# Kernel tuning notes

Measured on AMD Instinct MI355X. Metric: run time of the kernel, lower is better.

Reference implementation:

```python
import jax, jax.numpy as jnp
import numpy as np

N = 100000          # nodes
E = 3200000         # edges (avg degree 32)
EPS = 1e-5          # BatchNorm eps
SLOPE = 0.01        # LeakyReLU negative slope


def _glorot(key, shape):
    lim = float(np.sqrt(6.0 / (shape[0] + shape[1])))
    return jax.random.uniform(key, shape, jnp.float32, -lim, lim)


def setup_inputs() -> dict:
    key = jax.random.key(0)
    ks = jax.random.split(key, 8)
    x = jax.random.normal(ks[0], (N, 128), jnp.float32)
    edge_index = jax.random.randint(ks[1], (2, E), 0, N, dtype=jnp.int64)
    W1 = _glorot(ks[2], (128, 256)); b1 = jnp.zeros((256,), jnp.float32)
    W2 = _glorot(ks[3], (256, 512)); b2 = jnp.zeros((512,), jnp.float32)
    g1 = jnp.ones((256,), jnp.float32); be1 = jnp.zeros((256,), jnp.float32)
    g2 = jnp.ones((512,), jnp.float32); be2 = jnp.zeros((512,), jnp.float32)
    Wd1 = _glorot(ks[4], (512, 4096)); bd1 = jnp.zeros((4096,), jnp.float32)
    Wd2 = _glorot(ks[5], (4096, 6)); bd2 = jnp.zeros((6,), jnp.float32)
    return dict(x=x, edge_index=edge_index, W1=W1, b1=b1, W2=W2, b2=b2,
                g1=g1, be1=be1, g2=g2, be2=be2,
                Wd1=Wd1, bd1=bd1, Wd2=Wd2, bd2=bd2)


def gcn_conv(x, src, dst, W, b):
    # PyG GCNConv: x' = D^{-1/2} (A + I) D^{-1/2} (x W) + b
    n = x.shape[0]
    xw = x @ W                                   # [N, out]
    loop = jnp.arange(n, dtype=src.dtype)
    s = jnp.concatenate([src, loop])             # add self-loops
    d = jnp.concatenate([dst, loop])
    deg = jax.ops.segment_sum(jnp.ones_like(d, dtype=x.dtype), d, num_segments=n)
    dinv = jnp.where(deg > 0, jax.lax.rsqrt(deg), 0.0)
    norm = dinv[s] * dinv[d]                     # [E+N]
    out = jax.ops.segment_sum(xw[s] * norm[:, None], d, num_segments=n)
    return out + b


def batchnorm(x, g, b):
    # training-mode BN over node dim, biased variance (as torch)
    m = x.mean(axis=0)
    v = x.var(axis=0)
    return (x - m) * jax.lax.rsqrt(v + EPS) * g + b


def leaky_relu(x):
    return jnp.where(x >= 0, x, SLOPE * x)


def reference(x, edge_index, W1, b1, W2, b2, g1, be1, g2, be2, Wd1, bd1, Wd2, bd2):
    src, dst = edge_index[0], edge_index[1]
    y = leaky_relu(batchnorm(gcn_conv(x, src, dst, W1, b1), g1, be1))
    y = leaky_relu(batchnorm(gcn_conv(y, src, dst, W2, b2), g2, be2))
    y = leaky_relu(y @ Wd1 + bd1)
    y = y @ Wd2 + bd2
    return jax.nn.softmax(y, axis=1)
```

## Files before the change

### kernel.cpp

```cpp
#include <hip/hip_runtime.h>
#include <math.h>

#define LEAKY(t) ((t) >= 0.0f ? (t) : 0.01f * (t))

typedef __attribute__((ext_vector_type(8))) short bf16x8;
typedef __attribute__((ext_vector_type(4))) float f32x4;

static __device__ __forceinline__ float b2f(unsigned short u) {
    return __uint_as_float(((unsigned)u) << 16);
}
static __device__ __forceinline__ unsigned short f2b(float f) {
    unsigned x = __float_as_uint(f);
    unsigned r = (x + 0x7fffu + ((x >> 16) & 1u)) >> 16;
    return (unsigned short)r;
}


__global__ void k_seti(int* __restrict__ p, int v, int n) {
    int i = blockIdx.x * blockDim.x + threadIdx.x;
    int st = gridDim.x * blockDim.x;
    for (; i < n; i += st) p[i] = v;
}

__global__ void k_setf(float* __restrict__ p, float v, int n) {
    int i = blockIdx.x * blockDim.x + threadIdx.x;
    int st = gridDim.x * blockDim.x;
    for (; i < n; i += st) p[i] = v;
}

__global__ void k_stash_b16(const unsigned short* __restrict__ a, int i0, int i1, int i2, int i3,
                            float* __restrict__ dst) {
    if (threadIdx.x == 0 && blockIdx.x == 0) {
        dst[0] = b2f(a[i0]); dst[1] = b2f(a[i1]); dst[2] = b2f(a[i2]); dst[3] = b2f(a[i3]);
    }
}


__global__ void k_cvt(const float* __restrict__ src, unsigned short* __restrict__ dst,
                      long long n4) {
    long long i = (long long)blockIdx.x * blockDim.x + threadIdx.x;
    long long st = (long long)gridDim.x * blockDim.x;
    for (; i < n4; i += st) {
        float4 v = *(const float4*)(src + 4 * i);
        ushort4 o;
        o.x = f2b(v.x); o.y = f2b(v.y); o.z = f2b(v.z); o.w = f2b(v.w);
        *(ushort4*)(dst + 4 * i) = o;
    }
}


__global__ void k_detect(const int* __restrict__ ei, int* __restrict__ flag) {
    __shared__ int nz;
    if (threadIdx.x == 0) nz = 0;
    __syncthreads();
    int acc = 0;
    for (int i = threadIdx.x; i < 1024; i += 256) acc |= ei[2 * i + 1];
    if (acc != 0) atomicOr(&nz, 1);
    __syncthreads();
    if (threadIdx.x == 0) *flag = (nz == 0) ? 1 : 0;
}


__global__ void k_count(const int* __restrict__ ei, int E, int Nn,
                        const int* __restrict__ flag, int* __restrict__ cnt) {
    int f = *flag;
    int i = blockIdx.x * blockDim.x + threadIdx.x;
    int stride = gridDim.x * blockDim.x;
    for (; i < E; i += stride) {
        int d = f ? ei[2 * E + 2 * i] : ei[E + i];
        if ((unsigned)d < (unsigned)Nn) atomicAdd(&cnt[d], 1);
    }
}

__global__ void k_dinv(const int* __restrict__ cnt, float* __restrict__ dinv, int n) {
    int i = blockIdx.x * blockDim.x + threadIdx.x;
    if (i < n) dinv[i] = rsqrtf((float)(cnt[i] + 1));
}

__global__ void k_scan(const int* __restrict__ cnt, int* __restrict__ start, int n) {
    __shared__ int sm[256];
    __shared__ int carry;
    int tid = threadIdx.x;
    if (tid == 0) carry = 0;
    __syncthreads();
    for (int base = 0; base < n; base += 1024) {
        int i0 = base + tid * 4;
        int v0 = (i0 + 0 < n) ? cnt[i0 + 0] : 0;
        int v1 = (i0 + 1 < n) ? cnt[i0 + 1] : 0;
        int v2 = (i0 + 2 < n) ? cnt[i0 + 2] : 0;
        int v3 = (i0 + 3 < n) ? cnt[i0 + 3] : 0;
        int s = v0 + v1 + v2 + v3;
        sm[tid] = s;
        __syncthreads();
        int x = s;
        for (int off = 1; off < 256; off <<= 1) {
            int y = (tid >= off) ? sm[tid - off] : 0;
            __syncthreads();
            x += y;
            sm[tid] = x;
            __syncthreads();
        }
        int e = x - s + carry;
        if (i0 + 0 < n) start[i0 + 0] = e; e += v0;
        if (i0 + 1 < n) start[i0 + 1] = e; e += v1;
        if (i0 + 2 < n) start[i0 + 2] = e; e += v2;
        if (i0 + 3 < n) start[i0 + 3] = e; e += v3;
        __syncthreads();
        if (tid == 255) carry += sm[255];
        __syncthreads();
    }
    if (tid == 0) start[n] = carry;
}

__global__ void k_copy_i32(const int* __restrict__ a, int* __restrict__ b, int n) {
    int i = blockIdx.x * blockDim.x + threadIdx.x;
    if (i < n) b[i] = a[i];
}

__global__ void k_fill(const int* __restrict__ ei, int E, int Nn,
                       const int* __restrict__ flag,
                       int* __restrict__ cursor, int* __restrict__ srcS) {
    int f = *flag;
    int i = blockIdx.x * blockDim.x + threadIdx.x;
    int stride = gridDim.x * blockDim.x;
    for (; i < E; i += stride) {
        int s = f ? ei[2 * i] : ei[i];
        int d = f ? ei[2 * E + 2 * i] : ei[E + i];
        if ((unsigned)d < (unsigned)Nn) {
            int p = atomicAdd(&cursor[d], 1);
            srcS[p] = ((unsigned)s < (unsigned)Nn) ? s : 0;
        }
    }
}


__global__ void k_aggb(const unsigned short* __restrict__ X, const float* __restrict__ dinv,
                       const int* __restrict__ start, const int* __restrict__ srcS,
                       unsigned short* __restrict__ out, int F, int M) {
    int t = threadIdx.x;
    for (int n = blockIdx.x; n < M; n += gridDim.x) {
        float di = dinv[n];
        unsigned v = *(const unsigned*)(X + (size_t)n * F + 2 * t);
        float a0 = b2f((unsigned short)(v & 0xffff)) * di;
        float a1 = b2f((unsigned short)(v >> 16)) * di;
        int j = start[n], e1 = start[n + 1];
        for (; j + 1 < e1; j += 2) {
            int s0 = srcS[j], s1 = srcS[j + 1];
            float w0 = dinv[s0], w1 = dinv[s1];
            unsigned u0 = *(const unsigned*)(X + (size_t)s0 * F + 2 * t);
            unsigned u1 = *(const unsigned*)(X + (size_t)s1 * F + 2 * t);
            a0 += b2f((unsigned short)(u0 & 0xffff)) * w0;
            a1 += b2f((unsigned short)(u0 >> 16)) * w0;
            a0 += b2f((unsigned short)(u1 & 0xffff)) * w1;
            a1 += b2f((unsigned short)(u1 >> 16)) * w1;
        }
        if (j < e1) {
            int s0 = srcS[j];
            float w0 = dinv[s0];
            unsigned u0 = *(const unsigned*)(X + (size_t)s0 * F + 2 * t);
            a0 += b2f((unsigned short)(u0 & 0xffff)) * w0;
            a1 += b2f((unsigned short)(u0 >> 16)) * w0;
        }
        unsigned o = (unsigned)f2b(a0 * di) | ((unsigned)f2b(a1 * di) << 16);
        *(unsigned*)(out + (size_t)n * F + 2 * t) = o;
    }
}


__global__ __launch_bounds__(256, 2)
void k_gemm1(const unsigned short* __restrict__ A, const unsigned short* __restrict__ W1s,
             unsigned short* __restrict__ C, int M) {
    int tid = threadIdx.x;
    int lane = tid & 63, w = tid >> 6;
    int lr = lane & 15, lg = lane >> 4;
    int row0 = blockIdx.x * 64;
    int arow = row0 + w * 16 + lr;
    const unsigned short* Ar = A + (size_t)(arow < M ? arow : (M - 1)) * 128;
    bf16x8 a8[4];
#pragma unroll
    for (int ko = 0; ko < 4; ko++)
        a8[ko] = *(const bf16x8*)(Ar + ko * 32 + lg * 8);
    for (int ct = 0; ct < 16; ct += 2) {
        f32x4 acc0 = {0.f, 0.f, 0.f, 0.f}, acc1 = {0.f, 0.f, 0.f, 0.f};
#pragma unroll
        for (int ko = 0; ko < 4; ko++) {
            const unsigned short* bp = W1s + ((size_t)(ct * 4 + ko) * 64 + lane) * 8;
            bf16x8 b0 = *(const bf16x8*)bp;
            bf16x8 b1 = *(const bf16x8*)(bp + 2048);
            acc0 = __builtin_amdgcn_mfma_f32_16x16x32_bf16(a8[ko], b0, acc0, 0, 0, 0);
            acc1 = __builtin_amdgcn_mfma_f32_16x16x32_bf16(a8[ko], b1, acc1, 0, 0, 0);
        }
        int col = ct * 16 + lr;
#pragma unroll
        for (int i = 0; i < 4; i++) {
            int r = row0 + w * 16 + lg * 4 + i;
            if (r < M) {
                C[(size_t)r * 256 + col] = f2b(acc0[i]);
                C[(size_t)r * 256 + col + 16] = f2b(acc1[i]);
            }
        }
    }
}


__global__ void k_gemm2stats(const unsigned short* __restrict__ T2,
                             const unsigned short* __restrict__ W2s,
                             float* __restrict__ sums, int M) {
    __shared__ float ls[512];
    __shared__ float lq[512];
    int tid = threadIdx.x;
    int lane = tid & 63, w = tid >> 6;
    int lr = lane & 15, lg = lane >> 4;
    int row0 = blockIdx.x * 64;
    for (int i = tid; i < 512; i += 256) { ls[i] = 0.f; lq[i] = 0.f; }
    __syncthreads();

    int arow = row0 + w * 16 + lr;
    bf16x8 a8[8];
    if (arow < M) {
        const unsigned short* T2r = T2 + (size_t)arow * 256;
#pragma unroll
        for (int ko = 0; ko < 8; ko++)
            a8[ko] = *(const bf16x8*)(T2r + ko * 32 + lg * 8);
    } else {
#pragma unroll
        for (int ko = 0; ko < 8; ko++)
            a8[ko] = (bf16x8){0, 0, 0, 0, 0, 0, 0, 0};
    }

    for (int ct = 0; ct < 32; ct += 2) {
        f32x4 acc0 = {0.f, 0.f, 0.f, 0.f}, acc1 = {0.f, 0.f, 0.f, 0.f};
#pragma unroll
        for (int ko = 0; ko < 8; ko++) {
            const unsigned short* bp = W2s + ((size_t)(ct * 8 + ko) * 64 + lane) * 8;
            bf16x8 b0 = *(const bf16x8*)bp;
            bf16x8 b1 = *(const bf16x8*)(bp + 4096);
            acc0 = __builtin_amdgcn_mfma_f32_16x16x32_bf16(a8[ko], b0, acc0, 0, 0, 0);
            acc1 = __builtin_amdgcn_mfma_f32_16x16x32_bf16(a8[ko], b1, acc1, 0, 0, 0);
        }
        float s0 = 0.f, q0 = 0.f, s1 = 0.f, q1 = 0.f;
#pragma unroll
        for (int i = 0; i < 4; i++) {
            float y0 = acc0[i]; s0 += y0; q0 += y0 * y0;
            float y1 = acc1[i]; s1 += y1; q1 += y1 * y1;
        }
        s0 += __shfl_xor(s0, 16); s0 += __shfl_xor(s0, 32);
        q0 += __shfl_xor(q0, 16); q0 += __shfl_xor(q0, 32);
        s1 += __shfl_xor(s1, 16); s1 += __shfl_xor(s1, 32);
        q1 += __shfl_xor(q1, 16); q1 += __shfl_xor(q1, 32);
        if (lg == 0) {
            atomicAdd(&ls[ct * 16 + lr], s0);
            atomicAdd(&lq[ct * 16 + lr], q0);
            atomicAdd(&ls[(ct + 1) * 16 + lr], s1);
            atomicAdd(&lq[(ct + 1) * 16 + lr], q1);
        }
    }
    __syncthreads();
    for (int c = tid; c < 512; c += 256) {
        atomicAdd(&sums[c], ls[c]);
        atomicAdd(&sums[512 + c], lq[c]);
    }
}


__global__ void k_bnparam(float* __restrict__ sums, const float* __restrict__ g,
                          const float* __restrict__ be, int n, int F) {
    int c = blockIdx.x * blockDim.x + threadIdx.x;
    if (c < F) {
        float m = sums[c] / n;
        float v = sums[F + c] / n - m * m;
        float a = g[c] * rsqrtf(v + 1e-5f);
        sums[c] = a;
        sums[F + c] = be[c] - m * a;
    }
}

__global__ void k_colstats_b16(const unsigned short* __restrict__ X, float* __restrict__ sums, int n) {
    int t = threadIdx.x;
    int r0 = blockIdx.x * 256;
    int r1 = min(r0 + 256, n);
    float s = 0.f, q = 0.f;
    for (int r = r0; r < r1; r++) {
        float v = b2f(X[(size_t)r * 256 + t]);
        s += v; q += v * v;
    }
    atomicAdd(&sums[t], s);
    atomicAdd(&sums[256 + t], q);
}

__global__ void k_bnleaky_b16(unsigned short* __restrict__ X, const float* __restrict__ p,
                              long long total) {
    long long i = (long long)blockIdx.x * blockDim.x + threadIdx.x;
    long long stride = (long long)gridDim.x * blockDim.x;
    for (; i < total; i += stride) {
        int c = (int)(i & 255);
        float y = b2f(X[i]) * p[c] + p[256 + c];
        X[i] = f2b(LEAKY(y));
    }
}


__global__ void k_swz(const float* __restrict__ src, unsigned short* __restrict__ dst,
                      int N, int KO) {
    __shared__ float t[32][65];
    int tid = threadIdx.x;
    int ko = blockIdx.x;
    int n0 = blockIdx.y * 64;
    int r = tid >> 3, c8 = (tid & 7) * 8;
    const float* s = src + (size_t)(ko * 32 + r) * N + n0 + c8;
    float4 v0 = *(const float4*)s;
    float4 v1 = *(const float4*)(s + 4);
    t[r][c8 + 0] = v0.x; t[r][c8 + 1] = v0.y; t[r][c8 + 2] = v0.z; t[r][c8 + 3] = v0.w;
    t[r][c8 + 4] = v1.x; t[r][c8 + 5] = v1.y; t[r][c8 + 6] = v1.z; t[r][c8 + 7] = v1.w;
    __syncthreads();
    int cc = tid >> 6, lane = tid & 63;
    int lr = lane & 15, lg = lane >> 4;
    int ct = (n0 >> 4) + cc;
    bf16x8 ov;
#pragma unroll
    for (int j = 0; j < 8; j++) ov[j] = (short)f2b(t[lg * 8 + j][cc * 16 + lr]);
    *(bf16x8*)(dst + ((size_t)(ct * KO + ko) * 64 + lane) * 8) = ov;
}


__global__ __launch_bounds__(256, 2)
void k_dense(const unsigned short* __restrict__ T2,
             const unsigned short* __restrict__ W2s,
             const float* __restrict__ bnp,
             const float* __restrict__ bd1,
             const unsigned short* __restrict__ Wd1s,
             const float* __restrict__ Wd2,
             float* __restrict__ logits, int M) {
    __shared__ unsigned short Y2[64][520];
    __shared__ float sl[2][64][6];
    int tid = threadIdx.x;
    int lane = tid & 63, w = tid >> 6;
    int lr = lane & 15, lg = lane >> 4;
    int row0 = blockIdx.x * 64;

    int arow = row0 + w * 16 + lr;
    const unsigned short* T2r = T2 + (size_t)(arow < M ? arow : (M - 1)) * 256;
    bf16x8 a8[8];
#pragma unroll
    for (int ko = 0; ko < 8; ko++)
        a8[ko] = *(const bf16x8*)(T2r + ko * 32 + lg * 8);
    for (int ct = 0; ct < 32; ct += 2) {
        f32x4 acc0 = {0.f, 0.f, 0.f, 0.f}, acc1 = {0.f, 0.f, 0.f, 0.f};
#pragma unroll
        for (int ko = 0; ko < 8; ko++) {
            const unsigned short* bp = W2s + ((size_t)(ct * 8 + ko) * 64 + lane) * 8;
            bf16x8 b0 = *(const bf16x8*)bp;
            bf16x8 b1 = *(const bf16x8*)(bp + 4096);
            acc0 = __builtin_amdgcn_mfma_f32_16x16x32_bf16(a8[ko], b0, acc0, 0, 0, 0);
            acc1 = __builtin_amdgcn_mfma_f32_16x16x32_bf16(a8[ko], b1, acc1, 0, 0, 0);
        }
        int col = ct * 16 + lr;
        float sc0 = bnp[col], sh0 = bnp[512 + col];
        float sc1 = bnp[col + 16], sh1 = bnp[512 + col + 16];
#pragma unroll
        for (int i = 0; i < 4; i++) {
            float y0 = fmaf(acc0[i], sc0, sh0); y0 = LEAKY(y0);
            Y2[w * 16 + lg * 4 + i][col] = f2b(y0);
            float y1 = fmaf(acc1[i], sc1, sh1); y1 = LEAKY(y1);
            Y2[w * 16 + lg * 4 + i][col + 16] = f2b(y1);
        }
    }
    __syncthreads();

    int rg = w & 1, ch = w >> 1;
    const unsigned short* rowA = &Y2[rg * 32 + lr][0];
    const unsigned short* rowB = &Y2[rg * 32 + 16 + lr][0];
    int co = lg * 8;
    bf16x8 pA0 = *(const bf16x8*)(rowA + 0 * 32 + co),  pB0 = *(const bf16x8*)(rowB + 0 * 32 + co);
    bf16x8 pA1 = *(const bf16x8*)(rowA + 1 * 32 + co),  pB1 = *(const bf16x8*)(rowB + 1 * 32 + co);
    bf16x8 pA2 = *(const bf16x8*)(rowA + 2 * 32 + co),  pB2 = *(const bf16x8*)(rowB + 2 * 32 + co);
    bf16x8 pA3 = *(const bf16x8*)(rowA + 3 * 32 + co),  pB3 = *(const bf16x8*)(rowB + 3 * 32 + co);
    bf16x8 pA4 = *(const bf16x8*)(rowA + 4 * 32 + co),  pB4 = *(const bf16x8*)(rowB + 4 * 32 + co);
    bf16x8 pA5 = *(const bf16x8*)(rowA + 5 * 32 + co),  pB5 = *(const bf16x8*)(rowB + 5 * 32 + co);
    bf16x8 pA6 = *(const bf16x8*)(rowA + 6 * 32 + co),  pB6 = *(const bf16x8*)(rowB + 6 * 32 + co);
    bf16x8 pA7 = *(const bf16x8*)(rowA + 7 * 32 + co),  pB7 = *(const bf16x8*)(rowB + 7 * 32 + co);
    bf16x8 pA8 = *(const bf16x8*)(rowA + 8 * 32 + co),  pB8 = *(const bf16x8*)(rowB + 8 * 32 + co);
    bf16x8 pA9 = *(const bf16x8*)(rowA + 9 * 32 + co),  pB9 = *(const bf16x8*)(rowB + 9 * 32 + co);
    bf16x8 pA10 = *(const bf16x8*)(rowA + 10 * 32 + co), pB10 = *(const bf16x8*)(rowB + 10 * 32 + co);
    bf16x8 pA11 = *(const bf16x8*)(rowA + 11 * 32 + co), pB11 = *(const bf16x8*)(rowB + 11 * 32 + co);
    bf16x8 pA12 = *(const bf16x8*)(rowA + 12 * 32 + co), pB12 = *(const bf16x8*)(rowB + 12 * 32 + co);
    bf16x8 pA13 = *(const bf16x8*)(rowA + 13 * 32 + co), pB13 = *(const bf16x8*)(rowB + 13 * 32 + co);
    bf16x8 pA14 = *(const bf16x8*)(rowA + 14 * 32 + co), pB14 = *(const bf16x8*)(rowB + 14 * 32 + co);
    bf16x8 pA15 = *(const bf16x8*)(rowA + 15 * 32 + co), pB15 = *(const bf16x8*)(rowB + 15 * 32 + co);

    float l0[4][6] = {{0.f}}, l1[4][6] = {{0.f}};
    int ct0 = ch * 128;
    for (int ct = ct0; ct < ct0 + 128; ++ct) {
        f32x4 acc0 = {0.f, 0.f, 0.f, 0.f}, acc1 = {0.f, 0.f, 0.f, 0.f};
        const unsigned short* bp = Wd1s + ((size_t)(ct * 16) * 64 + lane) * 8;
#define DSTEP(K, PA, PB) { bf16x8 b = *(const bf16x8*)(bp + (K) * 512); \
        acc0 = __builtin_amdgcn_mfma_f32_16x16x32_bf16(PA, b, acc0, 0, 0, 0); \
        acc1 = __builtin_amdgcn_mfma_f32_16x16x32_bf16(PB, b, acc1, 0, 0, 0); }
        DSTEP(0, pA0, pB0)   DSTEP(1, pA1, pB1)   DSTEP(2, pA2, pB2)   DSTEP(3, pA3, pB3)
        DSTEP(4, pA4, pB4)   DSTEP(5, pA5, pB5)   DSTEP(6, pA6, pB6)   DSTEP(7, pA7, pB7)
        DSTEP(8, pA8, pB8)   DSTEP(9, pA9, pB9)   DSTEP(10, pA10, pB10) DSTEP(11, pA11, pB11)
        DSTEP(12, pA12, pB12) DSTEP(13, pA13, pB13) DSTEP(14, pA14, pB14) DSTEP(15, pA15, pB15)
#undef DSTEP
        int col = ct * 16 + lr;
        float bv = bd1[col];
        const float* w2r = Wd2 + (size_t)col * 6;
        float u0 = w2r[0], u1 = w2r[1], u2 = w2r[2];
        float u3 = w2r[3], u4 = w2r[4], u5 = w2r[5];
#pragma unroll
        for (int i = 0; i < 4; i++) {
            float t0 = acc0[i] + bv; t0 = LEAKY(t0);
            l0[i][0] = fmaf(t0, u0, l0[i][0]);
            l0[i][1] = fmaf(t0, u1, l0[i][1]);
            l0[i][2] = fmaf(t0, u2, l0[i][2]);
            l0[i][3] = fmaf(t0, u3, l0[i][3]);
            l0[i][4] = fmaf(t0, u4, l0[i][4]);
            l0[i][5] = fmaf(t0, u5, l0[i][5]);
            float t1 = acc1[i] + bv; t1 = LEAKY(t1);
            l1[i][0] = fmaf(t1, u0, l1[i][0]);
            l1[i][1] = fmaf(t1, u1, l1[i][1]);
            l1[i][2] = fmaf(t1, u2, l1[i][2]);
            l1[i][3] = fmaf(t1, u3, l1[i][3]);
            l1[i][4] = fmaf(t1, u4, l1[i][4]);
            l1[i][5] = fmaf(t1, u5, l1[i][5]);
        }
    }
#pragma unroll
    for (int i = 0; i < 4; i++) {
#pragma unroll
        for (int o = 0; o < 6; o++) {
            float v0 = l0[i][o];
            v0 += __shfl_xor(v0, 1); v0 += __shfl_xor(v0, 2);
            v0 += __shfl_xor(v0, 4); v0 += __shfl_xor(v0, 8);
            float v1 = l1[i][o];
            v1 += __shfl_xor(v1, 1); v1 += __shfl_xor(v1, 2);
            v1 += __shfl_xor(v1, 4); v1 += __shfl_xor(v1, 8);
            if (lr == 0) {
                sl[ch][rg * 32 + lg * 4 + i][o] = v0;
                sl[ch][rg * 32 + 16 + lg * 4 + i][o] = v1;
            }
        }
    }
    __syncthreads();
    for (int i = tid; i < 384; i += 256) {
        int r = i / 6, o = i - r * 6;
        if (row0 + r < M)
            logits[(size_t)(row0 + r) * 6 + o] = sl[0][r][o] + sl[1][r][o];
    }
}


__global__ void k_softmax(const float* __restrict__ logits, const float* __restrict__ bd2,
                          float* __restrict__ out, int M) {
    int n = blockIdx.x * blockDim.x + threadIdx.x;
    if (n >= M) return;
    float l[6];
    float mx = -1e30f;
#pragma unroll
    for (int o = 0; o < 6; o++) {
        l[o] = logits[(size_t)n * 6 + o] + bd2[o];
        mx = fmaxf(mx, l[o]);
    }
    float s = 0.f;
#pragma unroll
    for (int o = 0; o < 6; o++) { l[o] = expf(l[o] - mx); s += l[o]; }
    float inv = 1.f / s;
#pragma unroll
    for (int o = 0; o < 6; o++) out[(size_t)n * 6 + o] = l[o] * inv;
}


__global__ void k_diag_ws(float* __restrict__ out, unsigned long long ws) {
    if (threadIdx.x == 0 && blockIdx.x == 0) {
        float f = (float)((double)ws / 1099511627776.0);
        if (f > 0.999f) f = 0.999f;
        out[0] = ldexpf(1.0f + f, 34);
    }
}

__global__ void k_diag(const int* __restrict__ eflag, const int* __restrict__ startM,
                       int E, const float* __restrict__ stash,
                       const float* __restrict__ logits, float* __restrict__ out) {
    if (threadIdx.x != 0 || blockIdx.x != 0) return;
    int b1 = *eflag;
    int b2 = (*startM == E) ? 1 : 0;
    int b3 = (fabsf(stash[0] - stash[1]) > 1e-12f || fabsf(stash[2] - stash[3]) > 1e-12f) ? 1 : 0;
    int b4 = (fabsf(stash[4]) > 1e-12f || fabsf(stash[5]) > 1e-12f ||
              fabsf(stash[6]) > 1e-12f || fabsf(stash[7]) > 1e-12f) ? 1 : 0;
    float d0 = fabsf(logits[0] - logits[6]);
    float d1 = fabsf(logits[0] - logits[1]);
    int b5 = (d0 > 1e-12f && d1 > 1e-12f) ? 1 : 0;
    if (b2 && b3 && b4 && b5) return;
    float meanabs = 0.f;
    for (int i = 0; i < 16; i++) meanabs += fabsf(logits[i]);
    meanabs *= (1.f / 16.f);
    int m = (int)(32.f + 8.f * log2f(meanabs + 1e-30f));
    m = m < 0 ? 0 : (m > 127 ? 127 : m);
    int Ee = 96 + 16 * b1 + 8 * b2 + 4 * b3 + 2 * b4 + b5;
    out[0] = ldexpf(1.0f + (float)m / 128.0f, Ee - 30);
}


extern "C" void kernel_launch(void* const* d_in, const int* in_sizes, int n_in,
                              void* d_out, int out_size, void* d_ws, size_t ws_size,
                              hipStream_t stream) {
    const float* x   = (const float*)d_in[0];
    const int*   ei  = (const int*)d_in[1];
    const float* W1  = (const float*)d_in[2];
    const float* W2  = (const float*)d_in[4];
    const float* g1  = (const float*)d_in[6];
    const float* be1 = (const float*)d_in[7];
    const float* g2  = (const float*)d_in[8];
    const float* be2 = (const float*)d_in[9];
    const float* Wd1 = (const float*)d_in[10];
    const float* bd1 = (const float*)d_in[11];
    const float* Wd2 = (const float*)d_in[12];
    const float* bd2 = (const float*)d_in[13];
    float* out = (float*)d_out;

    const int M = in_sizes[0] / 128;
    const int E = in_sizes[1] / 2;

    size_t szA = (size_t)M * 512;
    size_t szB = (size_t)M * 512;
    size_t csr = (size_t)M * 8 + ((size_t)M + 1) * 8 + (size_t)E * 4 + 8192 + 128 + 66000;
    size_t need = szA + szB + csr;

    if (ws_size < need) {
        k_setf<<<2048, 256, 0, stream>>>(out, 0.f, out_size);
        k_diag_ws<<<1, 64, 0, stream>>>(out, (unsigned long long)ws_size);
        return;
    }

    char* base = (char*)d_ws;
    unsigned short* xb  = (unsigned short*)base;
    unsigned short* T1b = (unsigned short*)base + (size_t)M * 128;
    unsigned short* T2  = (unsigned short*)base;
    unsigned short* Y1 = (unsigned short*)(base + szA);
    float* logits = (float*)(base + szA);
    unsigned short* W2s  = (unsigned short*)(base + szA + (size_t)8 * 1024 * 1024);
    unsigned short* Wd1s = (unsigned short*)(base + szA + (size_t)12 * 1024 * 1024);
    char* cb = base + szA + szB;
    float* dinv   = (float*)cb;
    int*   cnt    = (int*)(dinv + M);
    int*   startA = cnt + M;
    int*   cursor = startA + (M + 1);
    int*   srcS   = cursor + (M + 1);
    float* sums   = (float*)(srcS + E);
    int*   eflag  = (int*)(sums + 2048);
    float* stash  = (float*)(eflag + 8);
    unsigned short* W1s = (unsigned short*)(((uintptr_t)(stash + 16) + 63) & ~(uintptr_t)63);

    int mt  = (M + 63) / 64;
    int nb  = (M + 255) / 256;

    k_detect<<<1, 256, 0, stream>>>(ei, eflag);
    k_seti<<<2048, 256, 0, stream>>>(cnt, 0, M);
    k_count<<<4096, 256, 0, stream>>>(ei, E, M, eflag, cnt);
    k_dinv<<<nb, 256, 0, stream>>>(cnt, dinv, M);
    k_scan<<<1, 256, 0, stream>>>(cnt, startA, M);
    k_copy_i32<<<nb, 256, 0, stream>>>(startA, cursor, M);
    k_fill<<<4096, 256, 0, stream>>>(ei, E, M, eflag, cursor, srcS);
    k_cvt<<<2048, 256, 0, stream>>>(x, xb, (long long)M * 32);
    k_swz<<<dim3(4, 4), 256, 0, stream>>>(W1, W1s, 256, 4);

    k_aggb<<<8192, 64, 0, stream>>>(xb, dinv, startA, srcS, T1b, 128, M);
    k_stash_b16<<<1, 64, 0, stream>>>(T1b, 3, 128 * 7 + 3, 1, 128 * 7, stash);
    k_gemm1<<<mt, 256, 0, stream>>>(T1b, W1s, Y1, M);
    k_setf<<<8, 256, 0, stream>>>(sums, 0.f, 2048);
    k_colstats_b16<<<nb, 256, 0, stream>>>(Y1, sums, M);
    k_bnparam<<<1, 256, 0, stream>>>(sums, g1, be1, M, 256);
    k_bnleaky_b16<<<4096, 256, 0, stream>>>(Y1, sums, (long long)M * 256);
    k_stash_b16<<<1, 64, 0, stream>>>(Y1, 5, 77, 256 + 5, 256 * 9 + 5, stash + 4);

    k_aggb<<<4096, 128, 0, stream>>>(Y1, dinv, startA, srcS, T2, 256, M);
    k_swz<<<dim3(8, 8), 256, 0, stream>>>(W2, W2s, 512, 8);
    k_swz<<<dim3(16, 64), 256, 0, stream>>>(Wd1, Wd1s, 4096, 16);
    k_setf<<<8, 256, 0, stream>>>(sums, 0.f, 2048);
    k_gemm2stats<<<mt, 256, 0, stream>>>(T2, W2s, sums, M);
    k_bnparam<<<2, 256, 0, stream>>>(sums, g2, be2, M, 512);

    k_dense<<<mt, 256, 0, stream>>>(T2, W2s, sums, bd1, Wd1s, Wd2, logits, M);
    k_softmax<<<nb, 256, 0, stream>>>(logits, bd2, out, M);

    k_diag<<<1, 64, 0, stream>>>(eflag, startA + M, E, stash, logits, out);
}
```

Measured before the change: 2.624 ms.

## Stream Y2 fragments from LDS per k-step and compute four column tiles per pass

The intermediate Y2 tile is now stored in LDS in MFMA fragment order. The Wd1 stage reads A fragments from LDS inside the k-loop instead of holding all 32 fragments in registers. Each iteration now computes four 16-column output tiles, so each A fragment read is reused across four B tiles and there is more independent MFMA work in flight. This lowers register pressure and may help occupancy and latency hiding. The cost is extra LDS reads per k-step, a larger shared buffer (64 KB versus about 66 KB before, roughly the same), and more accumulators live at once.

```diff
diff --git a/kernel.cpp b/kernel.cpp
--- a/kernel.cpp
+++ b/kernel.cpp
@@ -331,7 +331,7 @@
              const unsigned short* __restrict__ Wd1s,
              const float* __restrict__ Wd2,
              float* __restrict__ logits, int M) {
-    __shared__ unsigned short Y2[64][520];
+    __shared__ unsigned short Y2f[4 * 8192];
     __shared__ float sl[2][64][6];
     int tid = threadIdx.x;
     int lane = tid & 63, w = tid >> 6;
@@ -357,72 +357,77 @@
         int col = ct * 16 + lr;
         float sc0 = bnp[col], sh0 = bnp[512 + col];
         float sc1 = bnp[col + 16], sh1 = bnp[512 + col + 16];
+        int koa = ct >> 1;
+        int lgb = lr >> 3;
+        int jj = lr & 7;
+        int base = w * 8192 + (koa * 64 + lgb * 16) * 8 + jj;
 #pragma unroll
         for (int i = 0; i < 4; i++) {
+            int r16 = lg * 4 + i;
             float y0 = fmaf(acc0[i], sc0, sh0); y0 = LEAKY(y0);
-            Y2[w * 16 + lg * 4 + i][col] = f2b(y0);
+            Y2f[base + r16 * 8] = f2b(y0);
             float y1 = fmaf(acc1[i], sc1, sh1); y1 = LEAKY(y1);
-            Y2[w * 16 + lg * 4 + i][col + 16] = f2b(y1);
+            Y2f[base + (32 * 8) + r16 * 8] = f2b(y1);
         }
     }
     __syncthreads();
 
     int rg = w & 1, ch = w >> 1;
-    const unsigned short* rowA = &Y2[rg * 32 + lr][0];
-    const unsigned short* rowB = &Y2[rg * 32 + 16 + lr][0];
-    int co = lg * 8;
-    bf16x8 pA0 = *(const bf16x8*)(rowA + 0 * 32 + co),  pB0 = *(const bf16x8*)(rowB + 0 * 32 + co);
-    bf16x8 pA1 = *(const bf16x8*)(rowA + 1 * 32 + co),  pB1 = *(const bf16x8*)(rowB + 1 * 32 + co);
-    bf16x8 pA2 = *(const bf16x8*)(rowA + 2 * 32 + co),  pB2 = *(const bf16x8*)(rowB + 2 * 32 + co);
-    bf16x8 pA3 = *(const bf16x8*)(rowA + 3 * 32 + co),  pB3 = *(const bf16x8*)(rowB + 3 * 32 + co);
-    bf16x8 pA4 = *(const bf16x8*)(rowA + 4 * 32 + co),  pB4 = *(const bf16x8*)(rowB + 4 * 32 + co);
-    bf16x8 pA5 = *(const bf16x8*)(rowA + 5 * 32 + co),  pB5 = *(const bf16x8*)(rowB + 5 * 32 + co);
-    bf16x8 pA6 = *(const bf16x8*)(rowA + 6 * 32 + co),  pB6 = *(const bf16x8*)(rowB + 6 * 32 + co);
-    bf16x8 pA7 = *(const bf16x8*)(rowA + 7 * 32 + co),  pB7 = *(const bf16x8*)(rowB + 7 * 32 + co);
-    bf16x8 pA8 = *(const bf16x8*)(rowA + 8 * 32 + co),  pB8 = *(const bf16x8*)(rowB + 8 * 32 + co);
-    bf16x8 pA9 = *(const bf16x8*)(rowA + 9 * 32 + co),  pB9 = *(const bf16x8*)(rowB + 9 * 32 + co);
-    bf16x8 pA10 = *(const bf16x8*)(rowA + 10 * 32 + co), pB10 = *(const bf16x8*)(rowB + 10 * 32 + co);
-    bf16x8 pA11 = *(const bf16x8*)(rowA + 11 * 32 + co), pB11 = *(const bf16x8*)(rowB + 11 * 32 + co);
-    bf16x8 pA12 = *(const bf16x8*)(rowA + 12 * 32 + co), pB12 = *(const bf16x8*)(rowB + 12 * 32 + co);
-    bf16x8 pA13 = *(const bf16x8*)(rowA + 13 * 32 + co), pB13 = *(const bf16x8*)(rowB + 13 * 32 + co);
-    bf16x8 pA14 = *(const bf16x8*)(rowA + 14 * 32 + co), pB14 = *(const bf16x8*)(rowB + 14 * 32 + co);
-    bf16x8 pA15 = *(const bf16x8*)(rowA + 15 * 32 + co), pB15 = *(const bf16x8*)(rowB + 15 * 32 + co);
-
+    const unsigned short* fA = Y2f + (size_t)(2 * rg) * 8192;
+    const unsigned short* fB = Y2f + (size_t)(2 * rg + 1) * 8192;
     float l0[4][6] = {{0.f}}, l1[4][6] = {{0.f}};
     int ct0 = ch * 128;
-    for (int ct = ct0; ct < ct0 + 128; ++ct) {
-        f32x4 acc0 = {0.f, 0.f, 0.f, 0.f}, acc1 = {0.f, 0.f, 0.f, 0.f};
-        const unsigned short* bp = Wd1s + ((size_t)(ct * 16) * 64 + lane) * 8;
-#define DSTEP(K, PA, PB) { bf16x8 b = *(const bf16x8*)(bp + (K) * 512); \
-        acc0 = __builtin_amdgcn_mfma_f32_16x16x32_bf16(PA, b, acc0, 0, 0, 0); \
-        acc1 = __builtin_amdgcn_mfma_f32_16x16x32_bf16(PB, b, acc1, 0, 0, 0); }
-        DSTEP(0, pA0, pB0)   DSTEP(1, pA1, pB1)   DSTEP(2, pA2, pB2)   DSTEP(3, pA3, pB3)
-        DSTEP(4, pA4, pB4)   DSTEP(5, pA5, pB5)   DSTEP(6, pA6, pB6)   DSTEP(7, pA7, pB7)
-        DSTEP(8, pA8, pB8)   DSTEP(9, pA9, pB9)   DSTEP(10, pA10, pB10) DSTEP(11, pA11, pB11)
-        DSTEP(12, pA12, pB12) DSTEP(13, pA13, pB13) DSTEP(14, pA14, pB14) DSTEP(15, pA15, pB15)
-#undef DSTEP
-        int col = ct * 16 + lr;
-        float bv = bd1[col];
-        const float* w2r = Wd2 + (size_t)col * 6;
-        float u0 = w2r[0], u1 = w2r[1], u2 = w2r[2];
-        float u3 = w2r[3], u4 = w2r[4], u5 = w2r[5];
-#pragma unroll
-        for (int i = 0; i < 4; i++) {
-            float t0 = acc0[i] + bv; t0 = LEAKY(t0);
-            l0[i][0] = fmaf(t0, u0, l0[i][0]);
-            l0[i][1] = fmaf(t0, u1, l0[i][1]);
-            l0[i][2] = fmaf(t0, u2, l0[i][2]);
-            l0[i][3] = fmaf(t0, u3, l0[i][3]);
-            l0[i][4] = fmaf(t0, u4, l0[i][4]);
-            l0[i][5] = fmaf(t0, u5, l0[i][5]);
-            float t1 = acc1[i] + bv; t1 = LEAKY(t1);
-            l1[i][0] = fmaf(t1, u0, l1[i][0]);
-            l1[i][1] = fmaf(t1, u1, l1[i][1]);
-            l1[i][2] = fmaf(t1, u2, l1[i][2]);
-            l1[i][3] = fmaf(t1, u3, l1[i][3]);
-            l1[i][4] = fmaf(t1, u4, l1[i][4]);
-            l1[i][5] = fmaf(t1, u5, l1[i][5]);
-        }
+    for (int ct = ct0; ct < ct0 + 128; ct += 4) {
+        f32x4 aA0 = {0.f, 0.f, 0.f, 0.f}, aA1 = {0.f, 0.f, 0.f, 0.f};
+        f32x4 aA2 = {0.f, 0.f, 0.f, 0.f}, aA3 = {0.f, 0.f, 0.f, 0.f};
+        f32x4 aB0 = {0.f, 0.f, 0.f, 0.f}, aB1 = {0.f, 0.f, 0.f, 0.f};
+        f32x4 aB2 = {0.f, 0.f, 0.f, 0.f}, aB3 = {0.f, 0.f, 0.f, 0.f};
+#pragma unroll
+        for (int ko = 0; ko < 16; ko++) {
+            const unsigned short* bp = Wd1s + ((size_t)(ct * 16 + ko) * 64 + lane) * 8;
+            bf16x8 b0 = *(const bf16x8*)bp;
+            bf16x8 b1 = *(const bf16x8*)(bp + 8192);
+            bf16x8 b2 = *(const bf16x8*)(bp + 16384);
+            bf16x8 b3 = *(const bf16x8*)(bp + 24576);
+            bf16x8 pa = *(const bf16x8*)(fA + (ko * 64 + lane) * 8);
+            aA0 = __builtin_amdgcn_mfma_f32_16x16x32_bf16(pa, b0, aA0, 0, 0, 0);
+            aA1 = __builtin_amdgcn_mfma_f32_16x16x32_bf16(pa, b1, aA1, 0, 0, 0);
+            aA2 = __builtin_amdgcn_mfma_f32_16x16x32_bf16(pa, b2, aA2, 0, 0, 0);
+            aA3 = __builtin_amdgcn_mfma_f32_16x16x32_bf16(pa, b3, aA3, 0, 0, 0);
+            bf16x8 pb = *(const bf16x8*)(fB + (ko * 64 + lane) * 8);
+            aB0 = __builtin_amdgcn_mfma_f32_16x16x32_bf16(pb, b0, aB0, 0, 0, 0);
+            aB1 = __builtin_amdgcn_mfma_f32_16x16x32_bf16(pb, b1, aB1, 0, 0, 0);
+            aB2 = __builtin_amdgcn_mfma_f32_16x16x32_bf16(pb, b2, aB2, 0, 0, 0);
+            aB3 = __builtin_amdgcn_mfma_f32_16x16x32_bf16(pb, b3, aB3, 0, 0, 0);
+        }
+#define EPI(C, AA, BB) { \
+        int col = (ct + (C)) * 16 + lr; \
+        float bv = bd1[col]; \
+        const float* w2r = Wd2 + (size_t)col * 6; \
+        float u0 = w2r[0], u1 = w2r[1], u2 = w2r[2]; \
+        float u3 = w2r[3], u4 = w2r[4], u5 = w2r[5]; \
+        _Pragma("unroll") \
+        for (int i = 0; i < 4; i++) { \
+            float t0 = AA[i] + bv; t0 = LEAKY(t0); \
+            l0[i][0] = fmaf(t0, u0, l0[i][0]); \
+            l0[i][1] = fmaf(t0, u1, l0[i][1]); \
+            l0[i][2] = fmaf(t0, u2, l0[i][2]); \
+            l0[i][3] = fmaf(t0, u3, l0[i][3]); \
+            l0[i][4] = fmaf(t0, u4, l0[i][4]); \
+            l0[i][5] = fmaf(t0, u5, l0[i][5]); \
+            float t1 = BB[i] + bv; t1 = LEAKY(t1); \
+            l1[i][0] = fmaf(t1, u0, l1[i][0]); \
+            l1[i][1] = fmaf(t1, u1, l1[i][1]); \
+            l1[i][2] = fmaf(t1, u2, l1[i][2]); \
+            l1[i][3] = fmaf(t1, u3, l1[i][3]); \
+            l1[i][4] = fmaf(t1, u4, l1[i][4]); \
+            l1[i][5] = fmaf(t1, u5, l1[i][5]); \
+        } }
+        EPI(0, aA0, aB0)
+        EPI(1, aA1, aB1)
+        EPI(2, aA2, aB2)
+        EPI(3, aA3, aB3)
+#undef EPI
     }
 #pragma unroll
     for (int i = 0; i < 4; i++) {
```

New measurement: 3.118 ms. 18.8% more time.
